# Performance work log

Measured on AMD Instinct MI355X. Metric: run time of the kernel, lower is better.

Reference implementation:

```python
import jax, jax.numpy as jnp
import numpy as np

B, T, D = 128, 2048, 256
LAMDA = 0.5


def setup_inputs() -> dict:
    key = jax.random.key(0)
    ks = jax.random.split(key, 8)
    return {
        "sentiment": jax.random.normal(ks[0], (B, D), jnp.float32),
        "aspect": jax.random.normal(ks[1], (B, D), jnp.float32),
        "sentiment_memory": jax.random.normal(ks[2], (B, T, D), jnp.float32),
        "aspect_memory": jax.random.normal(ks[3], (B, T, D), jnp.float32),
        "mask": jnp.ones((B, T), jnp.float32),
        # MultiplicativeAttention params: rand(D,D)*0.2-0.1, bias zeros(1)
        "W_mul": jax.random.uniform(ks[4], (D, D), jnp.float32) * 0.2 - 0.1,
        "b_mul": jnp.zeros((1,), jnp.float32),
        # AdditiveAttention: Linear(2D, 1) -> weight vector [2D], bias [1]
        "w_ss": jax.random.normal(ks[5], (2 * D,), jnp.float32) * 0.02,
        "b_ss": jnp.zeros((1,), jnp.float32),
        "w_sa": jax.random.normal(ks[6], (2 * D,), jnp.float32) * 0.02,
        "b_sa": jnp.zeros((1,), jnp.float32),
    }


def _masked_norm(scores, mask):
    # exp(scores - max) * mask, normalized (matches torch branch exactly)
    s = scores - jnp.max(scores, axis=1, keepdims=True)
    e = jnp.exp(s) * mask
    return e / jnp.sum(e, axis=1, keepdims=True)


def _additive_attn(query, key_mem, w, b, mask):
    # Linear([key; query_repeated]) == key @ w_k + query @ w_q + b
    d = query.shape[-1]
    scores = key_mem @ w[:d] + (query @ w[d:])[:, None] + b[0]  # [B,T]
    return _masked_norm(scores, mask)


def reference(sentiment, aspect, sentiment_memory, aspect_memory, mask,
              W_mul, b_mul, w_ss, b_ss, w_sa, b_sa):
    # Multiplicative attention over aspect_memory (no mask -> plain softmax)
    mids = aspect @ W_mul.T                                        # W @ q, [B,D]
    a_scores = jnp.tanh(jnp.einsum('btd,bd->bt', aspect_memory, mids) + b_mul[0])
    aspect_attn = jax.nn.softmax(a_scores, axis=1)                 # [B,T]
    new_aspect = jnp.einsum('bt,btd->bd', aspect_attn, aspect_memory)  # [B,D]

    ss_attn = _additive_attn(sentiment, sentiment_memory, w_ss, b_ss, mask)
    sa_attn = _additive_attn(new_aspect, sentiment_memory, w_sa, b_sa, mask)
    s_attn = (1.0 - LAMDA) * ss_attn + LAMDA * sa_attn             # [B,T]

    sentiment_out = jnp.einsum('bt,btd->bd', s_attn, sentiment_memory)[:, None, :]  # [B,1,D]
    aspect_out = aspect + new_aspect                                # [B,D]
    return sentiment_out, aspect_out
```

## Files before the change

### kernel.cpp

```cpp
#include <hip/hip_runtime.h>
#include <math.h>

#define BB 128
#define TT 2048
#define DD 256
#define SPLIT 8
#define ROWS_PER_BLOCK (TT / SPLIT)
#define WAVES 4
#define ROWS_PER_WAVE (ROWS_PER_BLOCK / WAVES)

#define WS_MIDS 0
#define WS_P1ACC (WS_MIDS + BB * DD)
#define WS_P1SUM (WS_P1ACC + BB * SPLIT * DD)
#define WS_P2ACC_SS (WS_P1SUM + BB * SPLIT)
#define WS_P2ACC_SA (WS_P2ACC_SS + BB * SPLIT * DD)
#define WS_P2SUM_SS (WS_P2ACC_SA + BB * SPLIT * DD)
#define WS_P2SUM_SA (WS_P2SUM_SS + BB * SPLIT)

__device__ __forceinline__ float dot4(const float4& a, const float4& b) {
    return a.x * b.x + a.y * b.y + a.z * b.z + a.w * b.w;
}

__device__ __forceinline__ float tanh_fast(float x) {
    float ax = fabsf(x);
    float t = __expf(-2.0f * ax);
    float th = (1.0f - t) / (1.0f + t);
    return copysignf(th, x);
}

__device__ __forceinline__ float red16(float v) {
    int t;
    t = __builtin_amdgcn_update_dpp(0, __float_as_int(v), 0xB1, 0xF, 0xF, true);
    v += __int_as_float(t);
    t = __builtin_amdgcn_update_dpp(0, __float_as_int(v), 0x4E, 0xF, 0xF, true);
    v += __int_as_float(t);
    t = __builtin_amdgcn_update_dpp(0, __float_as_int(v), 0x141, 0xF, 0xF, true);
    v += __int_as_float(t);
    t = __builtin_amdgcn_update_dpp(0, __float_as_int(v), 0x140, 0xF, 0xF, true);
    v += __int_as_float(t);
    return v;
}

__device__ __forceinline__ float xmerge(float v) {
    v += __shfl_xor(v, 16, 64);
    v += __shfl_xor(v, 32, 64);
    return v;
}
__device__ __forceinline__ void merge4(float4& a) {
    a.x = xmerge(a.x); a.y = xmerge(a.y);
    a.z = xmerge(a.z); a.w = xmerge(a.w);
}
__device__ __forceinline__ void fma4(float4& a, float s, const float4& v) {
    a.x = fmaf(s, v.x, a.x); a.y = fmaf(s, v.y, a.y);
    a.z = fmaf(s, v.z, a.z); a.w = fmaf(s, v.w, a.w);
}

__global__ __launch_bounds__(DD) void mids_kernel(
    const float* __restrict__ aspect, const float* __restrict__ W,
    float* __restrict__ ws)
{
    const int b = blockIdx.x;
    const int i = threadIdx.x;
    __shared__ float a[DD];
    a[i] = aspect[b * DD + i];
    __syncthreads();
    const float4* wrow = (const float4*)(W + (size_t)i * DD);
    float acc = 0.f;
    #pragma unroll 8
    for (int j4 = 0; j4 < DD / 4; ++j4) {
        float4 w4 = wrow[j4];
        acc += a[4 * j4 + 0] * w4.x + a[4 * j4 + 1] * w4.y +
               a[4 * j4 + 2] * w4.z + a[4 * j4 + 3] * w4.w;
    }
    ws[WS_MIDS + b * DD + i] = acc;
}

__global__ __launch_bounds__(256) void pass_kernel(
    const float* __restrict__ smem_g, const float* __restrict__ amem_g,
    const float* __restrict__ mask, const float* __restrict__ w_ss,
    const float* __restrict__ w_sa, const float* __restrict__ b_mul,
    float* __restrict__ ws)
{
    const int s = blockIdx.x;
    const int b = blockIdx.y;
    const int tid = threadIdx.x;
    const int wave = tid >> 6;
    const int lane = tid & 63;
    const int g = lane >> 4;
    const int sub = lane & 15;
    const int t0 = s * ROWS_PER_BLOCK + wave * ROWS_PER_WAVE;

    __shared__ __align__(16) float lds_acc[2 * WAVES * DD];
    __shared__ float lds_sum[2 * WAVES];

    if (blockIdx.z == 0) {
        const float4* mp = (const float4*)(ws + WS_MIDS + b * DD + sub * 16);
        const float4 m0 = mp[0], m1 = mp[1], m2 = mp[2], m3 = mp[3];
        const float bm = b_mul[0];
        const float* base = amem_g + ((size_t)b * TT + t0 + g) * DD + sub * 16;
        float4 a0 = make_float4(0.f,0.f,0.f,0.f), a1 = a0, a2 = a0, a3 = a0;
        float lsum = 0.f;
        for (int r = 0; r < ROWS_PER_WAVE; r += 4) {
            const float4* p = (const float4*)(base + (size_t)r * DD);
            float4 v0 = p[0], v1 = p[1], v2 = p[2], v3 = p[3];
            float pd = (dot4(v0, m0) + dot4(v1, m1)) +
                       (dot4(v2, m2) + dot4(v3, m3));
            float d = red16(pd);
            float e = __expf(tanh_fast(d + bm));
            lsum += e;
            fma4(a0, e, v0); fma4(a1, e, v1);
            fma4(a2, e, v2); fma4(a3, e, v3);
        }
        lsum = xmerge(lsum);
        merge4(a0); merge4(a1); merge4(a2); merge4(a3);
        if (g == 0) {
            float4* dst = (float4*)(lds_acc + wave * DD + sub * 16);
            dst[0] = a0; dst[1] = a1; dst[2] = a2; dst[3] = a3;
        }
        if (lane == 0) lds_sum[wave] = lsum;
        __syncthreads();
        float tot = lds_acc[0 * DD + tid] + lds_acc[1 * DD + tid] +
                    lds_acc[2 * DD + tid] + lds_acc[3 * DD + tid];
        ws[WS_P1ACC + (size_t)(b * SPLIT + s) * DD + tid] = tot;
        if (tid == 0)
            ws[WS_P1SUM + b * SPLIT + s] =
                lds_sum[0] + lds_sum[1] + lds_sum[2] + lds_sum[3];
    } else {
        const float4* wsp = (const float4*)(w_ss + sub * 16);
        const float4* wap = (const float4*)(w_sa + sub * 16);
        const float4 ws0 = wsp[0], ws1 = wsp[1], ws2 = wsp[2], ws3 = wsp[3];
        const float4 wa0 = wap[0], wa1 = wap[1], wa2 = wap[2], wa3 = wap[3];
        const float* base = smem_g + ((size_t)b * TT + t0 + g) * DD + sub * 16;
        const float* mrow = mask + (size_t)b * TT + t0 + g;
        float4 s0 = make_float4(0.f,0.f,0.f,0.f), s1 = s0, s2 = s0, s3 = s0;
        float4 q0 = s0, q1 = s0, q2 = s0, q3 = s0;
        float lss = 0.f, lsa = 0.f;
        for (int r = 0; r < ROWS_PER_WAVE; r += 4) {
            const float4* p = (const float4*)(base + (size_t)r * DD);
            float4 v0 = p[0], v1 = p[1], v2 = p[2], v3 = p[3];
            float m = mrow[r];
            float pds = (dot4(v0, ws0) + dot4(v1, ws1)) +
                        (dot4(v2, ws2) + dot4(v3, ws3));
            float pda = (dot4(v0, wa0) + dot4(v1, wa1)) +
                        (dot4(v2, wa2) + dot4(v3, wa3));
            float dss = red16(pds);
            float dsa = red16(pda);
            float ess = __expf(dss) * m;
            float esa = __expf(dsa) * m;
            lss += ess;
            lsa += esa;
            fma4(s0, ess, v0); fma4(s1, ess, v1);
            fma4(s2, ess, v2); fma4(s3, ess, v3);
            fma4(q0, esa, v0); fma4(q1, esa, v1);
            fma4(q2, esa, v2); fma4(q3, esa, v3);
        }
        lss = xmerge(lss);
        lsa = xmerge(lsa);
        merge4(s0); merge4(s1); merge4(s2); merge4(s3);
        merge4(q0); merge4(q1); merge4(q2); merge4(q3);
        if (g == 0) {
            float4* d1 = (float4*)(lds_acc + wave * DD + sub * 16);
            d1[0] = s0; d1[1] = s1; d1[2] = s2; d1[3] = s3;
            float4* d2 = (float4*)(lds_acc + (WAVES + wave) * DD + sub * 16);
            d2[0] = q0; d2[1] = q1; d2[2] = q2; d2[3] = q3;
        }
        if (lane == 0) {
            lds_sum[wave] = lss;
            lds_sum[WAVES + wave] = lsa;
        }
        __syncthreads();
        float tot_ss = lds_acc[0 * DD + tid] + lds_acc[1 * DD + tid] +
                       lds_acc[2 * DD + tid] + lds_acc[3 * DD + tid];
        float tot_sa = lds_acc[(WAVES + 0) * DD + tid] + lds_acc[(WAVES + 1) * DD + tid] +
                       lds_acc[(WAVES + 2) * DD + tid] + lds_acc[(WAVES + 3) * DD + tid];
        ws[WS_P2ACC_SS + (size_t)(b * SPLIT + s) * DD + tid] = tot_ss;
        ws[WS_P2ACC_SA + (size_t)(b * SPLIT + s) * DD + tid] = tot_sa;
        if (tid == 0) {
            ws[WS_P2SUM_SS + b * SPLIT + s] =
                lds_sum[0] + lds_sum[1] + lds_sum[2] + lds_sum[3];
            ws[WS_P2SUM_SA + b * SPLIT + s] =
                lds_sum[4] + lds_sum[5] + lds_sum[6] + lds_sum[7];
        }
    }
}

__global__ __launch_bounds__(DD) void combine_kernel(
    const float* __restrict__ aspect, const float* __restrict__ ws,
    float* __restrict__ out)
{
    const int b = blockIdx.x;
    const int d = threadIdx.x;
    if (blockIdx.y == 0) {
        float acc = 0.f, l = 0.f;
        #pragma unroll
        for (int s = 0; s < SPLIT; ++s)
            acc += ws[WS_P1ACC + (size_t)(b * SPLIT + s) * DD + d];
        #pragma unroll
        for (int s = 0; s < SPLIT; ++s)
            l += ws[WS_P1SUM + b * SPLIT + s];
        out[BB * DD + b * DD + d] = aspect[b * DD + d] + acc / l;
    } else {
        float ass = 0.f, asa = 0.f, lss = 0.f, lsa = 0.f;
        #pragma unroll
        for (int s = 0; s < SPLIT; ++s) {
            ass += ws[WS_P2ACC_SS + (size_t)(b * SPLIT + s) * DD + d];
            asa += ws[WS_P2ACC_SA + (size_t)(b * SPLIT + s) * DD + d];
        }
        #pragma unroll
        for (int s = 0; s < SPLIT; ++s) {
            lss += ws[WS_P2SUM_SS + b * SPLIT + s];
            lsa += ws[WS_P2SUM_SA + b * SPLIT + s];
        }
        out[b * DD + d] = 0.5f * (ass / lss) + 0.5f * (asa / lsa);
    }
}

extern "C" void kernel_launch(void* const* d_in, const int* in_sizes, int n_in,
                              void* d_out, int out_size, void* d_ws, size_t ws_size,
                              hipStream_t stream) {
    (void)in_sizes; (void)n_in; (void)out_size; (void)ws_size;
    const float* aspect = (const float*)d_in[1];
    const float* smem   = (const float*)d_in[2];
    const float* amem   = (const float*)d_in[3];
    const float* mask   = (const float*)d_in[4];
    const float* W_mul  = (const float*)d_in[5];
    const float* b_mul  = (const float*)d_in[6];
    const float* w_ss   = (const float*)d_in[7];
    const float* w_sa   = (const float*)d_in[9];
    float* out = (float*)d_out;
    float* ws  = (float*)d_ws;

    mids_kernel<<<BB, DD, 0, stream>>>(aspect, W_mul, ws);
    pass_kernel<<<dim3(SPLIT, BB, 2), 256, 0, stream>>>(
        smem, amem, mask, w_ss, w_sa, b_mul, ws);
    combine_kernel<<<dim3(BB, 2), DD, 0, stream>>>(aspect, ws, out);
}
```

Baseline: 537.5 us.

## Interleave column layout, register-prefetch rows, and run both passes per block

Each lane now reads float4 columns strided by 64 floats, so the 16 lanes of a row-group issue contiguous coalesced loads instead of each lane reading 16 consecutive floats. The next row's four float4 values are prefetched into registers to overlap memory latency with the dot/exp/fma work. The aspect pass and the sentiment pass now run sequentially in the same block, halving the grid, with an added barrier before LDS reuse. The intent is better load coalescing and latency hiding, at the cost of fewer blocks in flight and higher register pressure.

```diff
diff --git a/kernel.cpp b/kernel.cpp
--- a/kernel.cpp
+++ b/kernel.cpp
@@ -88,21 +88,30 @@
     const int lane = tid & 63;
     const int g = lane >> 4;
     const int sub = lane & 15;
-    const int t0 = s * ROWS_PER_BLOCK + wave * ROWS_PER_WAVE;
+    const int t0w = s * ROWS_PER_BLOCK + wave * ROWS_PER_WAVE;
 
     __shared__ __align__(16) float lds_acc[2 * WAVES * DD];
     __shared__ float lds_sum[2 * WAVES];
 
-    if (blockIdx.z == 0) {
-        const float4* mp = (const float4*)(ws + WS_MIDS + b * DD + sub * 16);
-        const float4 m0 = mp[0], m1 = mp[1], m2 = mp[2], m3 = mp[3];
+    {
+        const float4* mp = (const float4*)(ws + WS_MIDS + b * DD);
+        const float4 m0 = mp[0 * 16 + sub], m1 = mp[1 * 16 + sub],
+                     m2 = mp[2 * 16 + sub], m3 = mp[3 * 16 + sub];
         const float bm = b_mul[0];
-        const float* base = amem_g + ((size_t)b * TT + t0 + g) * DD + sub * 16;
+        const float* base = amem_g + ((size_t)b * TT + t0w + g) * DD + sub * 4;
         float4 a0 = make_float4(0.f,0.f,0.f,0.f), a1 = a0, a2 = a0, a3 = a0;
         float lsum = 0.f;
+        float4 v0 = *(const float4*)(base + 0);
+        float4 v1 = *(const float4*)(base + 64);
+        float4 v2 = *(const float4*)(base + 128);
+        float4 v3 = *(const float4*)(base + 192);
         for (int r = 0; r < ROWS_PER_WAVE; r += 4) {
-            const float4* p = (const float4*)(base + (size_t)r * DD);
-            float4 v0 = p[0], v1 = p[1], v2 = p[2], v3 = p[3];
+            const int rn = (r + 4 < ROWS_PER_WAVE) ? (r + 4) : r;
+            const float* nb = base + (size_t)rn * DD;
+            float4 n0 = *(const float4*)(nb + 0);
+            float4 n1 = *(const float4*)(nb + 64);
+            float4 n2 = *(const float4*)(nb + 128);
+            float4 n3 = *(const float4*)(nb + 192);
             float pd = (dot4(v0, m0) + dot4(v1, m1)) +
                        (dot4(v2, m2) + dot4(v3, m3));
             float d = red16(pd);
@@ -110,12 +119,14 @@
             lsum += e;
             fma4(a0, e, v0); fma4(a1, e, v1);
             fma4(a2, e, v2); fma4(a3, e, v3);
+            v0 = n0; v1 = n1; v2 = n2; v3 = n3;
         }
         lsum = xmerge(lsum);
         merge4(a0); merge4(a1); merge4(a2); merge4(a3);
         if (g == 0) {
-            float4* dst = (float4*)(lds_acc + wave * DD + sub * 16);
-            dst[0] = a0; dst[1] = a1; dst[2] = a2; dst[3] = a3;
+            float4* dst = (float4*)(lds_acc + wave * DD);
+            dst[0 * 16 + sub] = a0; dst[1 * 16 + sub] = a1;
+            dst[2 * 16 + sub] = a2; dst[3 * 16 + sub] = a3;
         }
         if (lane == 0) lds_sum[wave] = lsum;
         __syncthreads();
@@ -125,19 +136,31 @@
         if (tid == 0)
             ws[WS_P1SUM + b * SPLIT + s] =
                 lds_sum[0] + lds_sum[1] + lds_sum[2] + lds_sum[3];
-    } else {
-        const float4* wsp = (const float4*)(w_ss + sub * 16);
-        const float4* wap = (const float4*)(w_sa + sub * 16);
-        const float4 ws0 = wsp[0], ws1 = wsp[1], ws2 = wsp[2], ws3 = wsp[3];
-        const float4 wa0 = wap[0], wa1 = wap[1], wa2 = wap[2], wa3 = wap[3];
-        const float* base = smem_g + ((size_t)b * TT + t0 + g) * DD + sub * 16;
-        const float* mrow = mask + (size_t)b * TT + t0 + g;
+    }
+
+    {
+        const float4* wsp = (const float4*)w_ss;
+        const float4* wap = (const float4*)w_sa;
+        const float4 ws0 = wsp[0 * 16 + sub], ws1 = wsp[1 * 16 + sub],
+                     ws2 = wsp[2 * 16 + sub], ws3 = wsp[3 * 16 + sub];
+        const float4 wa0 = wap[0 * 16 + sub], wa1 = wap[1 * 16 + sub],
+                     wa2 = wap[2 * 16 + sub], wa3 = wap[3 * 16 + sub];
+        const float* base = smem_g + ((size_t)b * TT + t0w + g) * DD + sub * 4;
+        const float* mrow = mask + (size_t)b * TT + t0w + g;
         float4 s0 = make_float4(0.f,0.f,0.f,0.f), s1 = s0, s2 = s0, s3 = s0;
         float4 q0 = s0, q1 = s0, q2 = s0, q3 = s0;
         float lss = 0.f, lsa = 0.f;
+        float4 v0 = *(const float4*)(base + 0);
+        float4 v1 = *(const float4*)(base + 64);
+        float4 v2 = *(const float4*)(base + 128);
+        float4 v3 = *(const float4*)(base + 192);
         for (int r = 0; r < ROWS_PER_WAVE; r += 4) {
-            const float4* p = (const float4*)(base + (size_t)r * DD);
-            float4 v0 = p[0], v1 = p[1], v2 = p[2], v3 = p[3];
+            const int rn = (r + 4 < ROWS_PER_WAVE) ? (r + 4) : r;
+            const float* nb = base + (size_t)rn * DD;
+            float4 n0 = *(const float4*)(nb + 0);
+            float4 n1 = *(const float4*)(nb + 64);
+            float4 n2 = *(const float4*)(nb + 128);
+            float4 n3 = *(const float4*)(nb + 192);
             float m = mrow[r];
             float pds = (dot4(v0, ws0) + dot4(v1, ws1)) +
                         (dot4(v2, ws2) + dot4(v3, ws3));
@@ -153,16 +176,20 @@
             fma4(s2, ess, v2); fma4(s3, ess, v3);
             fma4(q0, esa, v0); fma4(q1, esa, v1);
             fma4(q2, esa, v2); fma4(q3, esa, v3);
+            v0 = n0; v1 = n1; v2 = n2; v3 = n3;
         }
         lss = xmerge(lss);
         lsa = xmerge(lsa);
         merge4(s0); merge4(s1); merge4(s2); merge4(s3);
         merge4(q0); merge4(q1); merge4(q2); merge4(q3);
+        __syncthreads();
         if (g == 0) {
-            float4* d1 = (float4*)(lds_acc + wave * DD + sub * 16);
-            d1[0] = s0; d1[1] = s1; d1[2] = s2; d1[3] = s3;
-            float4* d2 = (float4*)(lds_acc + (WAVES + wave) * DD + sub * 16);
-            d2[0] = q0; d2[1] = q1; d2[2] = q2; d2[3] = q3;
+            float4* d1 = (float4*)(lds_acc + wave * DD);
+            d1[0 * 16 + sub] = s0; d1[1 * 16 + sub] = s1;
+            d1[2 * 16 + sub] = s2; d1[3 * 16 + sub] = s3;
+            float4* d2 = (float4*)(lds_acc + (WAVES + wave) * DD);
+            d2[0 * 16 + sub] = q0; d2[1 * 16 + sub] = q1;
+            d2[2 * 16 + sub] = q2; d2[3 * 16 + sub] = q3;
         }
         if (lane == 0) {
             lds_sum[wave] = lss;
@@ -231,7 +258,7 @@
     float* ws  = (float*)d_ws;
 
     mids_kernel<<<BB, DD, 0, stream>>>(aspect, W_mul, ws);
-    pass_kernel<<<dim3(SPLIT, BB, 2), 256, 0, stream>>>(
+    pass_kernel<<<dim3(SPLIT, BB), 256, 0, stream>>>(
         smem, amem, mask, w_ss, w_sa, b_mul, ws);
     combine_kernel<<<dim3(BB, 2), DD, 0, stream>>>(aspect, ws, out);
 }
```

Result: no change. 542.2 us (+0.9%).
